# Optimization experiments

Hardware: AMD Instinct MI355X
Metric: run time of the kernel (lower is better)

## Reference

```python
import jax, jax.numpy as jnp
import numpy as np

DIM = 14                     # input feature dim == log2(codebook_size)
NUM_CODEBOOKS = 1
CODEBOOK_DIM = DIM           # codebook_dim = log2(2**dim) = dim
CODEBOOK_SIZE = 2 ** DIM     # 16384
DIVERSITY_GAMMA = 1.0
ENTROPY_LOSS_WEIGHT = 0.1
COMMITMENT_LOSS_WEIGHT = 0.25
INV_TEMPERATURE = 100.0
EPS = 1e-5


def _entropy(p):
    # -sum p log p over last dim
    return -(p * jnp.log(jnp.clip(p, EPS))).sum(-1)


def _codebook():
    # all sign codes: bit j of code i -> +/-1, MSB-first mask 2**(d-1..0)
    codes = jnp.arange(CODEBOOK_SIZE, dtype=jnp.int32)[:, None]
    shifts = jnp.arange(CODEBOOK_DIM - 1, -1, -1, dtype=jnp.int32)
    bits = (codes >> shifts) & 1                       # [cs, d]
    return (bits * 2 - 1).astype(jnp.float32)          # [cs, d]


def setup_inputs() -> dict:
    key = jax.random.key(0)
    k1, k2, k3, k4, k5 = jax.random.split(key, 5)
    b, n = 4, 2048
    cdims = CODEBOOK_DIM * NUM_CODEBOOKS
    s = 1.0 / np.sqrt(DIM)
    return {
        "x": jax.random.normal(k1, (b, n, DIM), dtype=jnp.float32),
        "W_in": jax.random.uniform(k2, (cdims, DIM), jnp.float32, -s, s),
        "b_in": jax.random.uniform(k3, (cdims,), jnp.float32, -s, s),
        "W_out": jax.random.uniform(k4, (DIM, cdims), jnp.float32, -s, s),
        "b_out": jax.random.uniform(k5, (DIM,), jnp.float32, -s, s),
    }


def reference(x, W_in, b_in, W_out, b_out):
    b, n, _ = x.shape
    codebook = _codebook()                              # [cs, d]

    h = x @ W_in.T + b_in                               # [b, n, c*d]
    h = h.reshape(b, n, NUM_CODEBOOKS, CODEBOOK_DIM)    # [b, n, c, d]
    original_input = h

    # sign quantization (codebook_scale = 1.0)
    quantized = jnp.where(h > 0, 1.0, -1.0)
    # straight-through estimator (activation = identity)
    h_st = h + jax.lax.stop_gradient(quantized - h)

    # bitmask -> integer indices, MSB-first
    bit_mask = (2 ** jnp.arange(CODEBOOK_DIM - 1, -1, -1)).astype(jnp.int32)
    indices = ((h_st > 0).astype(jnp.int32) * bit_mask).sum(-1)  # [b, n, c]

    # entropy aux loss: prob over all 2**d codes
    # -distance = 2 * <orig, code>; softmax((-distance) * inv_temp)
    logits = (2.0 * INV_TEMPERATURE) * jnp.einsum(
        "bncd,jd->bncj", original_input, codebook)      # [b, n, c, cs]
    prob = jax.nn.softmax(logits, axis=-1)
    prob_flat = prob.reshape(b * n, NUM_CODEBOOKS, CODEBOOK_SIZE)

    per_sample_entropy = _entropy(prob_flat).mean()
    avg_prob = prob_flat.mean(0)                        # [c, cs]
    codebook_entropy = _entropy(avg_prob).mean()
    entropy_aux_loss = per_sample_entropy - DIVERSITY_GAMMA * codebook_entropy

    commit_loss = jnp.mean(
        (original_input - jax.lax.stop_gradient(quantized)) ** 2)

    out = h_st.reshape(b, n, NUM_CODEBOOKS * CODEBOOK_DIM) @ W_out.T + b_out

    indices = indices.squeeze(-1)  # keep_num_codebooks_dim False (c == 1)
    aux_loss = (entropy_aux_loss * ENTROPY_LOSS_WEIGHT
                + commit_loss * COMMITMENT_LOSS_WEIGHT)
    return out, indices, aux_loss
```

## Files before the change

### kernel.cpp

```cpp
#include <hip/hip_runtime.h>

#define NS 8192
#define D 14
#define CS 16384
#define NB 128
#define BT 64
#define FB 64
#define EPS 1e-5f
#define LNEPS (-11.512925464970229f)
#define THRESH 30.0f

__device__ __forceinline__ float waveRedSum(float v) {
    #pragma unroll
    for (int off = 32; off; off >>= 1) v += __shfl_xor(v, off);
    return v;
}

__global__ __launch_bounds__(BT) void lfq_main(
    const float* __restrict__ x, const float* __restrict__ Win,
    const float* __restrict__ bin, const float* __restrict__ Wout,
    const float* __restrict__ bout,
    float* __restrict__ out, float* __restrict__ idxOut,
    float* __restrict__ blockHist, float* __restrict__ entPart,
    float* __restrict__ commitPart, float* __restrict__ auxAcc,
    int* __restrict__ counter)
{
    __shared__ float shist[CS];
    __shared__ float sA[D * BT];
    __shared__ int   sB[D * BT];

    const int tid = threadIdx.x;
    const int b = blockIdx.x;
    const int i = b * BT + tid;

    float4* sh4 = (float4*)shist;
    #pragma unroll
    for (int u = 0; u < CS / 4 / BT; u++)
        sh4[u * BT + tid] = make_float4(0.f, 0.f, 0.f, 0.f);

    if (b == 0 && tid == 0) { auxAcc[0] = 0.f; counter[0] = 0; }

    float xv[D];
    #pragma unroll
    for (int k = 0; k < D; k++) xv[k] = x[i * D + k];

    float h[D];
    #pragma unroll
    for (int d = 0; d < D; d++) {
        float s = bin[d];
        #pragma unroll
        for (int k = 0; k < D; k++) s = fmaf(xv[k], Win[d * D + k], s);
        h[d] = s;
    }

    float q[D];
    int idx = 0;
    float commit = 0.f;
    #pragma unroll
    for (int d = 0; d < D; d++) {
        const bool pos = h[d] > 0.f;
        q[d] = pos ? 1.f : -1.f;
        idx |= (pos ? 1 : 0) << (13 - d);
        const float e = h[d] - q[d];
        commit = fmaf(e, e, commit);
    }

    #pragma unroll
    for (int e = 0; e < D; e++) {
        float s = bout[e];
        #pragma unroll
        for (int d = 0; d < D; d++) s = fmaf(q[d], Wout[e * D + d], s);
        out[i * D + e] = s;
    }
    idxOut[i] = (float)idx;

    int S = 0;
    float t0 = 0.f;
    #pragma unroll
    for (int d = 0; d < D; d++) {
        const float ab = fabsf(200.0f * h[d]);
        t0 -= __logf(1.0f + __expf(-2.f * ab));
        const float twoA = 2.f * ab;
        if (twoA < THRESH) {
            sA[S * BT + tid] = twoA;
            sB[S * BT + tid] = 1 << (13 - d);
            S++;
        }
    }

    __syncthreads();

    float ent;
    {
        const float p0 = __expf(t0);
        ent = p0 * fmaxf(t0, LNEPS);
        atomicAdd(&shist[idx], p0);
    }
    float tcur = t0;
    int jj = idx;
    const int total = 1 << S;
    for (int m = 1; m < total; m++) {
        const int k = __ffs(m) - 1;
        const int gn = m ^ (m >> 1);
        const float tw = sA[k * BT + tid];
        const int bm = sB[k * BT + tid];
        tcur += ((gn >> k) & 1) ? -tw : tw;
        jj ^= bm;
        const float p = __expf(tcur);
        ent = fmaf(p, fmaxf(tcur, LNEPS), ent);
        atomicAdd(&shist[jj], p);
    }

    const float es = waveRedSum(ent);
    const float cm = waveRedSum(commit);
    if (tid == 0) { entPart[b] = es; commitPart[b] = cm; }

    __syncthreads();

    float4* bh4 = (float4*)(blockHist + (size_t)b * CS);
    #pragma unroll
    for (int u = 0; u < CS / 4 / BT; u++)
        bh4[u * BT + tid] = sh4[u * BT + tid];
}

__global__ __launch_bounds__(256) void lfq_fold(
    const float* __restrict__ blockHist, const float* __restrict__ entPart,
    const float* __restrict__ commitPart, float* __restrict__ auxAcc,
    int* __restrict__ counter, float* __restrict__ aux)
{
    const int t = threadIdx.x;
    const int j = blockIdx.x * 256 + t;

    float s = 0.f;
    #pragma unroll 8
    for (int bb = 0; bb < NB; bb++) s += blockHist[(size_t)bb * CS + j];
    const float qv = s * (1.0f / NS);
    float cb = qv * __logf(fmaxf(qv, EPS));

    __shared__ float r[256];
    r[t] = cb;
    __syncthreads();
    #pragma unroll
    for (int st = 128; st > 0; st >>= 1) {
        if (t < st) r[t] += r[t + st];
        __syncthreads();
    }

    __shared__ int done;
    if (t == 0) {
        atomicAdd(auxAcc, r[0]);
        __threadfence();
        const int old = atomicAdd(counter, 1);
        done = (old == FB - 1) ? 1 : 0;
    }
    __syncthreads();

    if (done) {
        float es = (t < NB) ? entPart[t] : 0.f;
        float cm = (t < NB) ? commitPart[t] : 0.f;
        __shared__ float r2[256], r3[256];
        r2[t] = es; r3[t] = cm;
        __syncthreads();
        #pragma unroll
        for (int st = 128; st > 0; st >>= 1) {
            if (t < st) { r2[t] += r2[t + st]; r3[t] += r3[t + st]; }
            __syncthreads();
        }
        if (t == 0) {
            __threadfence();
            const float cbAll = atomicAdd(auxAcc, 0.0f);
            const float codebook_entropy = -cbAll;
            const float per_sample_entropy = -r2[0] / (float)NS;
            const float commit_loss = r3[0] / (float)(NS * D);
            const float entropy_aux = per_sample_entropy - codebook_entropy;
            aux[0] = entropy_aux * 0.1f + commit_loss * 0.25f;
        }
    }
}

extern "C" void kernel_launch(void* const* d_in, const int* in_sizes, int n_in,
                              void* d_out, int out_size, void* d_ws, size_t ws_size,
                              hipStream_t stream) {
    const float* x    = (const float*)d_in[0];
    const float* Win  = (const float*)d_in[1];
    const float* bin  = (const float*)d_in[2];
    const float* Wout = (const float*)d_in[3];
    const float* bout = (const float*)d_in[4];

    float* out    = (float*)d_out;
    float* idxOut = out + (size_t)NS * D;
    float* aux    = idxOut + NS;

    float* ws         = (float*)d_ws;
    float* blockHist  = ws;
    float* entPart    = blockHist + (size_t)NB * CS;
    float* commitPart = entPart + NB;
    float* auxAcc     = commitPart + NB;
    int*   counter    = (int*)(auxAcc + 1);

    lfq_main<<<NB, BT, 0, stream>>>(x, Win, bin, Wout, bout,
                                    out, idxOut, blockHist, entPart,
                                    commitPart, auxAcc, counter);
    lfq_fold<<<FB, 256, 0, stream>>>(blockHist, entPart, commitPart,
                                     auxAcc, counter, aux);
}
```

Baseline: 30.94 us.

## Replace per-block shared histograms with one global atomic histogram

Removes the 64KB per-block shared-memory histogram and the 8MB per-block histogram write-out. Each thread now does atomicAdd directly into a single global 16384-bin histogram, which a new zero kernel clears beforehand. The fold kernel then reads only one histogram instead of summing 128, and uses fewer blocks. This trades far less global traffic and lower LDS pressure for contended global float atomics and an extra kernel launch.

```diff
diff --git a/kernel.cpp b/kernel.cpp
--- a/kernel.cpp
+++ b/kernel.cpp
@@ -5,7 +5,7 @@
 #define CS 16384
 #define NB 128
 #define BT 64
-#define FB 64
+#define FB 16
 #define EPS 1e-5f
 #define LNEPS (-11.512925464970229f)
 #define THRESH 30.0f
@@ -16,29 +16,26 @@
     return v;
 }
 
+__global__ __launch_bounds__(256) void lfq_zero(
+    float* __restrict__ hist, float* __restrict__ auxAcc,
+    int* __restrict__ counter)
+{
+    ((float4*)hist)[blockIdx.x * 256 + threadIdx.x] =
+        make_float4(0.f, 0.f, 0.f, 0.f);
+    if (blockIdx.x == 0 && threadIdx.x == 0) { auxAcc[0] = 0.f; counter[0] = 0; }
+}
+
 __global__ __launch_bounds__(BT) void lfq_main(
     const float* __restrict__ x, const float* __restrict__ Win,
     const float* __restrict__ bin, const float* __restrict__ Wout,
     const float* __restrict__ bout,
     float* __restrict__ out, float* __restrict__ idxOut,
-    float* __restrict__ blockHist, float* __restrict__ entPart,
-    float* __restrict__ commitPart, float* __restrict__ auxAcc,
-    int* __restrict__ counter)
+    float* __restrict__ hist, float* __restrict__ entPart,
+    float* __restrict__ commitPart)
 {
-    __shared__ float shist[CS];
-    __shared__ float sA[D * BT];
-    __shared__ int   sB[D * BT];
-
     const int tid = threadIdx.x;
     const int b = blockIdx.x;
     const int i = b * BT + tid;
-
-    float4* sh4 = (float4*)shist;
-    #pragma unroll
-    for (int u = 0; u < CS / 4 / BT; u++)
-        sh4[u * BT + tid] = make_float4(0.f, 0.f, 0.f, 0.f);
-
-    if (b == 0 && tid == 0) { auxAcc[0] = 0.f; counter[0] = 0; }
 
     float xv[D];
     #pragma unroll
@@ -74,6 +71,8 @@
     }
     idxOut[i] = (float)idx;
 
+    __shared__ float sA[D * BT];
+    __shared__ int   sB[D * BT];
     int S = 0;
     float t0 = 0.f;
     #pragma unroll
@@ -88,13 +87,11 @@
         }
     }
 
-    __syncthreads();
-
     float ent;
     {
         const float p0 = __expf(t0);
         ent = p0 * fmaxf(t0, LNEPS);
-        atomicAdd(&shist[idx], p0);
+        atomicAdd(&hist[idx], p0);
     }
     float tcur = t0;
     int jj = idx;
@@ -108,34 +105,27 @@
         jj ^= bm;
         const float p = __expf(tcur);
         ent = fmaf(p, fmaxf(tcur, LNEPS), ent);
-        atomicAdd(&shist[jj], p);
+        atomicAdd(&hist[jj], p);
     }
 
     const float es = waveRedSum(ent);
     const float cm = waveRedSum(commit);
     if (tid == 0) { entPart[b] = es; commitPart[b] = cm; }
-
-    __syncthreads();
-
-    float4* bh4 = (float4*)(blockHist + (size_t)b * CS);
-    #pragma unroll
-    for (int u = 0; u < CS / 4 / BT; u++)
-        bh4[u * BT + tid] = sh4[u * BT + tid];
 }
 
 __global__ __launch_bounds__(256) void lfq_fold(
-    const float* __restrict__ blockHist, const float* __restrict__ entPart,
+    const float* __restrict__ hist, const float* __restrict__ entPart,
     const float* __restrict__ commitPart, float* __restrict__ auxAcc,
     int* __restrict__ counter, float* __restrict__ aux)
 {
     const int t = threadIdx.x;
-    const int j = blockIdx.x * 256 + t;
-
-    float s = 0.f;
-    #pragma unroll 8
-    for (int bb = 0; bb < NB; bb++) s += blockHist[(size_t)bb * CS + j];
-    const float qv = s * (1.0f / NS);
-    float cb = qv * __logf(fmaxf(qv, EPS));
+    const float4 v = ((const float4*)hist)[blockIdx.x * 256 + t];
+    float cb = 0.f;
+    #pragma unroll
+    for (int w = 0; w < 4; w++) {
+        const float qv = (&v.x)[w] * (1.0f / NS);
+        cb += qv * __logf(fmaxf(qv, EPS));
+    }
 
     __shared__ float r[256];
     r[t] = cb;
@@ -167,7 +157,6 @@
             __syncthreads();
         }
         if (t == 0) {
-            __threadfence();
             const float cbAll = atomicAdd(auxAcc, 0.0f);
             const float codebook_entropy = -cbAll;
             const float per_sample_entropy = -r2[0] / (float)NS;
@@ -192,15 +181,15 @@
     float* aux    = idxOut + NS;
 
     float* ws         = (float*)d_ws;
-    float* blockHist  = ws;
-    float* entPart    = blockHist + (size_t)NB * CS;
+    float* hist       = ws;
+    float* entPart    = hist + CS;
     float* commitPart = entPart + NB;
     float* auxAcc     = commitPart + NB;
     int*   counter    = (int*)(auxAcc + 1);
 
+    lfq_zero<<<FB, 256, 0, stream>>>(hist, auxAcc, counter);
     lfq_main<<<NB, BT, 0, stream>>>(x, Win, bin, Wout, bout,
-                                    out, idxOut, blockHist, entPart,
-                                    commitPart, auxAcc, counter);
-    lfq_fold<<<FB, 256, 0, stream>>>(blockHist, entPart, commitPart,
+                                    out, idxOut, hist, entPart, commitPart);
+    lfq_fold<<<FB, 256, 0, stream>>>(hist, entPart, commitPart,
                                      auxAcc, counter, aux);
 }
```

Result: faster. 27.24 us (-11.9%).
